# Performance work log

Measured on AMD Instinct MI355X. Metric: run time of the kernel, lower is better.

The kernel has to match this reference:

```python
import jax, jax.numpy as jnp
import numpy as np

B, N, NC, T, C, H = 8, 16, 16, 64, 512, 8


def setup_inputs() -> dict:
    key = jax.random.key(0)
    ks = jax.random.split(key, 7)
    s = 1.0 / np.sqrt(C)  # ~kaiming-uniform scale for Linear weights
    x = jax.random.normal(ks[0], (B, N, T, C), dtype=jnp.float32)
    c = jax.random.normal(ks[1], (B, NC, T, C), dtype=jnp.float32)
    mask = jax.random.randint(ks[2], (B, N * T, (N + NC) * T), 0, 2).astype(bool)
    Wq = jax.random.normal(ks[3], (C, C), dtype=jnp.float32) * s  # [out, in], torch Linear layout
    Wk = jax.random.normal(ks[4], (C, C), dtype=jnp.float32) * s
    Wv = jax.random.normal(ks[5], (C, C), dtype=jnp.float32) * s
    Wp = jax.random.normal(ks[6], (C, C), dtype=jnp.float32) * s
    return {"x": x, "c": c, "mask": mask, "Wq": Wq, "Wk": Wk, "Wv": Wv, "Wp": Wp}


def reference(x, c, mask, Wq, Wk, Wv, Wp):
    Bx, Nx, Tx, Cx = x.shape
    Dh = Cx // H
    kv_in = jnp.concatenate([x, c], axis=1)           # hybrid: [B, N+NC, T, C]
    Nk = kv_in.shape[1]
    # torch Linear: y = x @ W.T  -> einsum '...c,dc->...d'
    q = jnp.einsum('bntc,dc->bntd', x, Wq).reshape(Bx, Nx * Tx, H, Dh).transpose(0, 2, 1, 3)
    k = jnp.einsum('bntc,dc->bntd', kv_in, Wk).reshape(Bx, Nk * Tx, H, Dh).transpose(0, 2, 1, 3)
    v = jnp.einsum('bntc,dc->bntd', kv_in, Wv).reshape(Bx, Nk * Tx, H, Dh).transpose(0, 2, 1, 3)
    att = jnp.einsum('bhqd,bhkd->bhqk', q, k) * (1.0 / np.sqrt(Dh))  # [B,H,NT,NkT]
    att = jnp.where(mask[:, None, :, :], -jnp.inf, att)
    att = jax.nn.softmax(att, axis=-1)
    y = jnp.einsum('bhqk,bhkd->bhqd', att, v)          # [B,H,NT,Dh]
    y = y.transpose(0, 2, 1, 3).reshape(Bx, Nx * Tx, Cx)
    y = jnp.einsum('btc,dc->btd', y, Wp)
    return y.reshape(Bx, Nx, Tx, Cx)
```

## Files before the change

kernel.cpp:

```cpp
#include <hip/hip_runtime.h>
#include <hip/hip_bf16.h>
#include <stdint.h>

typedef __bf16 v8bf __attribute__((ext_vector_type(8)));
typedef short v4s __attribute__((ext_vector_type(4)));
typedef float f32x4 __attribute__((ext_vector_type(4)));

__device__ __forceinline__ void gload_lds16(const void* g, void* l) {
    __builtin_amdgcn_global_load_lds(
        (const __attribute__((address_space(1))) void*)g,
        (__attribute__((address_space(3))) void*)l, 16, 0, 0);
}

__device__ __forceinline__ unsigned short f2bf(float f) {
    __hip_bfloat16 h = __float2bfloat16(f);
    return __builtin_bit_cast(unsigned short, h);
}

__device__ __forceinline__ f32x4 mfma16x16x16bf(v4s a, v4s b, f32x4 c) {
#if __has_builtin(__builtin_amdgcn_mfma_f32_16x16x16bf16_1k)
    return __builtin_amdgcn_mfma_f32_16x16x16bf16_1k(a, b, c, 0, 0, 0);
#elif __has_builtin(__builtin_amdgcn_mfma_f32_16x16x16_bf16)
    return __builtin_amdgcn_mfma_f32_16x16x16_bf16(a, b, c, 0, 0, 0);
#else
    asm("s_nop 1\n\t"
        "v_mfma_f32_16x16x16_bf16 %0, %1, %2, %0\n\t"
        "s_nop 7\n\ts_nop 3"
        : "+v"(c) : "v"(a), "v"(b));
    return c;
#endif
}

__global__ __launch_bounds__(256) void cvt_xcw(const float* __restrict__ x,
                                               const float* __restrict__ c,
                                               const float* __restrict__ wq,
                                               const float* __restrict__ wk,
                                               const float* __restrict__ wv,
                                               const float* __restrict__ wp,
                                               __hip_bfloat16* __restrict__ xc,
                                               __hip_bfloat16* __restrict__ wout) {
    int bid = blockIdx.x;
    if (bid < 8192) {
        int i = bid * 256 + threadIdx.x;
        long e = (long)i * 4;
        int b = (int)(e >> 20);
        int rem = (int)(e & ((1 << 20) - 1));
        int r = rem >> 9;
        int col = rem & 511;
        const float* src = (r < 1024) ? (x + ((long)b << 19) + (long)r * 512 + col)
                                      : (c + ((long)b << 19) + (long)(r - 1024) * 512 + col);
        float4 v = *(const float4*)src;
        ushort4 o;
        o.x = f2bf(v.x); o.y = f2bf(v.y); o.z = f2bf(v.z); o.w = f2bf(v.w);
        ((ushort4*)xc)[i] = o;
    } else {
        int i = (bid - 8192) * 256 + threadIdx.x;
        int e = i * 4;
        int w = e >> 18;
        int off = e & ((1 << 18) - 1);
        const float* src = (w == 0 ? wq : w == 1 ? wk : w == 2 ? wv : wp) + off;
        float4 val = *(const float4*)src;
        ushort4 o;
        o.x = f2bf(val.x); o.y = f2bf(val.y); o.z = f2bf(val.z); o.w = f2bf(val.w);
        ((ushort4*)wout)[i] = o;
    }
}

__global__ __launch_bounds__(256) void cvt_mask(const int* __restrict__ mask,
                                                unsigned long long* __restrict__ mbt) {
    int t = threadIdx.x;
    long base = (long)blockIdx.x * 1024;
#pragma unroll
    for (int j = 0; j < 4; j++) {
        long i = base + j * 256 + t;
        int v = mask[i] != 0;
        unsigned long long bits = __ballot(v);
        if ((t & 63) == 0) {
            int b = (int)(i >> 21);
            int q = (int)((i >> 11) & 1023);
            int word = (int)((i >> 6) & 31);
            mbt[((long)b * 32 + word) * 1024 + q] = bits;
        }
    }
}

__global__ __launch_bounds__(256) void gemm_qkv(const __hip_bfloat16* __restrict__ A,
                                                const __hip_bfloat16* __restrict__ Bw,
                                                __hip_bfloat16* __restrict__ Qw,
                                                __hip_bfloat16* __restrict__ Kw,
                                                __hip_bfloat16* __restrict__ Vtw) {
    __shared__ union {
        struct { __hip_bfloat16 As[128 * 32]; __hip_bfloat16 Bs[128 * 32]; } s;
        __hip_bfloat16 T[128 * 136];
    } u;
    const int tid = threadIdx.x;
    const int wave = tid >> 6, lane = tid & 63;
    const int m0 = blockIdx.x * 128, n0 = blockIdx.y * 128;

    const int la = lane >> 2;
    const int kc = (lane & 3) * 8;
    const long ga0 = (long)(m0 + wave * 16 + la) * 512 + kc;
    const long ga1 = (long)(m0 + (wave + 4) * 16 + la) * 512 + kc;
    const long gb0 = (long)(n0 + wave * 16 + la) * 512 + kc;
    const long gb1 = (long)(n0 + (wave + 4) * 16 + la) * 512 + kc;

    f32x4 acc[4][4] = {};
    const int mw = (wave & 1) * 64, nw = (wave >> 1) * 64;
    const int lrow = lane & 15, lk = (lane >> 4) * 8;

    for (int k0 = 0; k0 < 512; k0 += 32) {
        gload_lds16(A + ga0 + k0, &u.s.As[wave * 512]);
        gload_lds16(A + ga1 + k0, &u.s.As[(wave + 4) * 512]);
        gload_lds16(Bw + gb0 + k0, &u.s.Bs[wave * 512]);
        gload_lds16(Bw + gb1 + k0, &u.s.Bs[(wave + 4) * 512]);
        __syncthreads();
        v8bf a[4], b[4];
#pragma unroll
        for (int i = 0; i < 4; i++) {
            a[i] = *(const v8bf*)&u.s.As[(mw + i * 16 + lrow) * 32 + lk];
            b[i] = *(const v8bf*)&u.s.Bs[(nw + i * 16 + lrow) * 32 + lk];
        }
#pragma unroll
        for (int mi = 0; mi < 4; mi++)
#pragma unroll
            for (int ni = 0; ni < 4; ni++)
                acc[mi][ni] = __builtin_amdgcn_mfma_f32_16x16x32_bf16(a[mi], b[ni], acc[mi][ni], 0, 0, 0);
        __syncthreads();
    }

    const int lq = lane >> 4;
    if (blockIdx.y < 8) {
#pragma unroll
        for (int mi = 0; mi < 4; mi++)
#pragma unroll
            for (int ni = 0; ni < 4; ni++)
#pragma unroll
                for (int r = 0; r < 4; r++) {
                    int grow = m0 + mw + mi * 16 + lq * 4 + r;
                    int gcol = n0 + nw + ni * 16 + lrow;
                    int w = gcol >> 9, g9 = gcol & 511;
                    int h = g9 >> 6, dh = g9 & 63;
                    int b_ = grow >> 11, rr = grow & 2047;
                    float val = acc[mi][ni][r];
                    if (w == 0) {
                        if (rr < 1024)
                            Qw[((long)(b_ * 8 + h) * 1024 + rr) * 64 + dh] =
                                __float2bfloat16(val * 0.1803368801f);
                    } else {
                        Kw[((long)(b_ * 8 + h) * 2048 + rr) * 64 + dh] = __float2bfloat16(val);
                    }
                }
    } else {
#pragma unroll
        for (int mi = 0; mi < 4; mi++)
#pragma unroll
            for (int ni = 0; ni < 4; ni++) {
                int n_l = nw + ni * 16 + lrow;
                int m_l = mw + mi * 16 + lq * 4;
                ushort4 pk;
                pk.x = f2bf(acc[mi][ni][0]); pk.y = f2bf(acc[mi][ni][1]);
                pk.z = f2bf(acc[mi][ni][2]); pk.w = f2bf(acc[mi][ni][3]);
                *(ushort4*)&u.T[n_l * 136 + m_l] = pk;
            }
        __syncthreads();
        const int no = (blockIdx.y - 8) * 128;
        const int b_ = m0 >> 11, rrb = m0 & 2047;
#pragma unroll
        for (int i = 0; i < 8; i++) {
            int s = tid + i * 256;
            int n_l = s >> 4, ch = s & 15;
            int ng = no + n_l;
            int h = ng >> 6, dh = ng & 63;
            uint4 v = *(const uint4*)&u.T[n_l * 136 + ch * 8];
            *(uint4*)&Vtw[((long)(b_ * 8 + h) * 64 + dh) * 2048 + rrb + ch * 8] = v;
        }
    }
}

__global__ __launch_bounds__(256) void gemm_out(const __hip_bfloat16* __restrict__ A,
                                                const __hip_bfloat16* __restrict__ Bw,
                                                float* __restrict__ outp) {
    __shared__ __hip_bfloat16 As[128 * 32];
    __shared__ __hip_bfloat16 Bs[128 * 32];
    const int tid = threadIdx.x;
    const int wave = tid >> 6, lane = tid & 63;
    const int m0 = blockIdx.x * 128, n0 = blockIdx.y * 128;

    const int la = lane >> 2;
    const int kc = (lane & 3) * 8;
    const long ga0 = (long)(m0 + wave * 16 + la) * 512 + kc;
    const long ga1 = (long)(m0 + (wave + 4) * 16 + la) * 512 + kc;
    const long gb0 = (long)(n0 + wave * 16 + la) * 512 + kc;
    const long gb1 = (long)(n0 + (wave + 4) * 16 + la) * 512 + kc;

    f32x4 acc[4][4] = {};
    const int mw = (wave & 1) * 64, nw = (wave >> 1) * 64;
    const int lrow = lane & 15, lk = (lane >> 4) * 8;

    for (int k0 = 0; k0 < 512; k0 += 32) {
        gload_lds16(A + ga0 + k0, &As[wave * 512]);
        gload_lds16(A + ga1 + k0, &As[(wave + 4) * 512]);
        gload_lds16(Bw + gb0 + k0, &Bs[wave * 512]);
        gload_lds16(Bw + gb1 + k0, &Bs[(wave + 4) * 512]);
        __syncthreads();
        v8bf a[4], b[4];
#pragma unroll
        for (int i = 0; i < 4; i++) {
            a[i] = *(const v8bf*)&As[(mw + i * 16 + lrow) * 32 + lk];
            b[i] = *(const v8bf*)&Bs[(nw + i * 16 + lrow) * 32 + lk];
        }
#pragma unroll
        for (int mi = 0; mi < 4; mi++)
#pragma unroll
            for (int ni = 0; ni < 4; ni++)
                acc[mi][ni] = __builtin_amdgcn_mfma_f32_16x16x32_bf16(a[mi], b[ni], acc[mi][ni], 0, 0, 0);
        __syncthreads();
    }

    const int lq = lane >> 4;
#pragma unroll
    for (int mi = 0; mi < 4; mi++)
#pragma unroll
        for (int ni = 0; ni < 4; ni++)
#pragma unroll
            for (int r = 0; r < 4; r++) {
                int grow = m0 + mw + mi * 16 + lq * 4 + r;
                int gcol = n0 + nw + ni * 16 + lrow;
                outp[(long)grow * 512 + gcol] = acc[mi][ni][r];
            }
}

__global__ __launch_bounds__(256) void flash(const __hip_bfloat16* __restrict__ Q,
                                             const __hip_bfloat16* __restrict__ K,
                                             const __hip_bfloat16* __restrict__ Vt,
                                             const unsigned long long* __restrict__ Mbt,
                                             __hip_bfloat16* __restrict__ Y) {
    constexpr int LDT = 72;
    __shared__ __hip_bfloat16 Ks[64 * LDT];
    __shared__ __hip_bfloat16 Vts[64 * LDT];

    const int L = blockIdx.x;
    const int b = L & 7, qt = (L >> 3) & 15, h = L >> 7;
    const int bh = b * 8 + h;
    const int tid = threadIdx.x, w = tid >> 6, lane = tid & 63;
    const int lcol = lane & 15, lq = lane >> 4;

    const __hip_bfloat16* Qp = Q + ((long)bh * 1024 + qt * 64 + w * 16 + lcol) * 64 + lq * 8;
    const __hip_bfloat16* Kg = K + (long)bh * 2048 * 64;
    const __hip_bfloat16* Vg = Vt + (long)bh * 64 * 2048;
    const unsigned long long* Mp = Mbt + (long)b * 32 * 1024 + qt * 64 + w * 16 + lcol;

    v8bf bq0 = *(const v8bf*)(Qp);
    v8bf bq1 = *(const v8bf*)(Qp + 32);

    f32x4 O[4] = {};
    float lsum = 0.f;

    for (int kt = 0; kt < 32; kt++) {
        unsigned long long mword = Mp[(long)kt * 1024];
        const uint4* ksrc = (const uint4*)(Kg + kt * 64 * 64);
#pragma unroll
        for (int i = 0; i < 2; i++) {
            int u = tid + i * 256, r = u >> 3, part = u & 7;
            *(uint4*)&Ks[r * LDT + part * 8] = ksrc[u];
        }
#pragma unroll
        for (int i = 0; i < 2; i++) {
            int u = tid + i * 256, dh = u >> 3, part = u & 7;
            *(uint4*)&Vts[dh * LDT + part * 8] = *(const uint4*)(Vg + (long)dh * 2048 + kt * 64 + part * 8);
        }
        __syncthreads();

#pragma unroll
        for (int nt = 0; nt < 4; nt++) {
            v8bf ak0 = *(const v8bf*)&Ks[(nt * 16 + lcol) * LDT + lq * 8];
            v8bf ak1 = *(const v8bf*)&Ks[(nt * 16 + lcol) * LDT + 32 + lq * 8];
            f32x4 st = {};
            st = __builtin_amdgcn_mfma_f32_16x16x32_bf16(ak0, bq0, st, 0, 0, 0);
            st = __builtin_amdgcn_mfma_f32_16x16x32_bf16(ak1, bq1, st, 0, 0, 0);
            unsigned int nib = (unsigned int)(mword >> (nt * 16 + lq * 4)) & 0xFu;
            float e0 = ((nib >> 0) & 1u) ? 0.f : __builtin_amdgcn_exp2f(fminf(st[0], 57.f));
            float e1 = ((nib >> 1) & 1u) ? 0.f : __builtin_amdgcn_exp2f(fminf(st[1], 57.f));
            float e2 = ((nib >> 2) & 1u) ? 0.f : __builtin_amdgcn_exp2f(fminf(st[2], 57.f));
            float e3 = ((nib >> 3) & 1u) ? 0.f : __builtin_amdgcn_exp2f(fminf(st[3], 57.f));
            lsum += (e0 + e1) + (e2 + e3);
            __hip_bfloat162 lo = __float22bfloat162_rn(make_float2(e0, e1));
            __hip_bfloat162 hi = __float22bfloat162_rn(make_float2(e2, e3));
            uint2 pku;
            __builtin_memcpy(&pku.x, &lo, 4);
            __builtin_memcpy(&pku.y, &hi, 4);
            v4s pa = __builtin_bit_cast(v4s, pku);
#pragma unroll
            for (int nd = 0; nd < 4; nd++) {
                v4s bv = *(const v4s*)&Vts[(nd * 16 + lcol) * LDT + nt * 16 + lq * 4];
                O[nd] = mfma16x16x16bf(pa, bv, O[nd]);
            }
        }
        __syncthreads();
    }

    float s = lsum;
    s += __shfl_xor(s, 16);
    s += __shfl_xor(s, 32);
    float inv[4];
#pragma unroll
    for (int r = 0; r < 4; r++) inv[r] = 1.f / __shfl(s, lq * 4 + r);

    __hip_bfloat16* Yp = Y + ((long)b * 1024 + qt * 64 + w * 16) * 512 + h * 64 + lcol;
#pragma unroll
    for (int nd = 0; nd < 4; nd++)
#pragma unroll
        for (int r = 0; r < 4; r++)
            Yp[(long)(lq * 4 + r) * 512 + nd * 16] = __float2bfloat16(O[nd][r] * inv[r]);
}

extern "C" void kernel_launch(void* const* d_in, const int* in_sizes, int n_in,
                              void* d_out, int out_size, void* d_ws, size_t ws_size,
                              hipStream_t stream) {
    const float* x = (const float*)d_in[0];
    const float* c = (const float*)d_in[1];
    const int* mask = (const int*)d_in[2];
    const float* Wq = (const float*)d_in[3];
    const float* Wk = (const float*)d_in[4];
    const float* Wv = (const float*)d_in[5];
    const float* Wp = (const float*)d_in[6];

    char* ws = (char*)d_ws;
    __hip_bfloat16* xc  = (__hip_bfloat16*)(ws);
    __hip_bfloat16* Wbf = (__hip_bfloat16*)(ws + 16777216);
    __hip_bfloat16* Qw  = (__hip_bfloat16*)(ws + 18874368);
    __hip_bfloat16* Kw  = (__hip_bfloat16*)(ws + 27262976);
    __hip_bfloat16* Vtw = (__hip_bfloat16*)(ws + 44040192);
    __hip_bfloat16* Yb  = (__hip_bfloat16*)(ws + 60817408);
    unsigned long long* Mbp = (unsigned long long*)(ws);

    cvt_xcw<<<9216, 256, 0, stream>>>(x, c, Wq, Wk, Wv, Wp, xc, Wbf);
    gemm_qkv<<<dim3(128, 12), 256, 0, stream>>>(xc, Wbf, Qw, Kw, Vtw);
    cvt_mask<<<16384, 256, 0, stream>>>(mask, Mbp);
    flash<<<1024, 256, 0, stream>>>(Qw, Kw, Vtw, Mbp, Yb);
    gemm_out<<<dim3(64, 4), 256, 0, stream>>>(Yb, Wbf + 3 * 262144, (float*)d_out);
}
```

Baseline: 285.7 us.

## Double-buffer K/V tiles in flash kernel with register prefetch and MFMA priority

Loads for the next K and V^T tile are issued into registers before computing on the current tile, then written to the alternate LDS buffer after compute, with one barrier per iteration instead of two. This aims to hide global-load latency behind the MFMA and exp work. It also wraps MFMA sections in s_setprio to favor matrix issue across waves. Costs are doubled LDS use and extra registers held across the loop, which may reduce occupancy.

```diff
diff --git a/kernel.cpp b/kernel.cpp
--- a/kernel.cpp
+++ b/kernel.cpp
@@ -236,8 +236,8 @@
                                              const unsigned long long* __restrict__ Mbt,
                                              __hip_bfloat16* __restrict__ Y) {
     constexpr int LDT = 72;
-    __shared__ __hip_bfloat16 Ks[64 * LDT];
-    __shared__ __hip_bfloat16 Vts[64 * LDT];
+    __shared__ __hip_bfloat16 Ks[2][64 * LDT];
+    __shared__ __hip_bfloat16 Vts[2][64 * LDT];
 
     const int L = blockIdx.x;
     const int b = L & 7, qt = (L >> 3) & 15, h = L >> 7;
@@ -250,34 +250,52 @@
     const __hip_bfloat16* Vg = Vt + (long)bh * 64 * 2048;
     const unsigned long long* Mp = Mbt + (long)b * 32 * 1024 + qt * 64 + w * 16 + lcol;
 
+    const int u0 = tid, u1 = tid + 256;
+    const int r0 = u0 >> 3, p0 = u0 & 7;
+    const int r1 = u1 >> 3, p1 = u1 & 7;
+
     v8bf bq0 = *(const v8bf*)(Qp);
     v8bf bq1 = *(const v8bf*)(Qp + 32);
 
     f32x4 O[4] = {};
     float lsum = 0.f;
 
+    {
+        const uint4* ksrc = (const uint4*)Kg;
+        uint4 k0 = ksrc[u0], k1 = ksrc[u1];
+        uint4 v0 = *(const uint4*)(Vg + (long)r0 * 2048 + p0 * 8);
+        uint4 v1 = *(const uint4*)(Vg + (long)r1 * 2048 + p1 * 8);
+        *(uint4*)&Ks[0][r0 * LDT + p0 * 8] = k0;
+        *(uint4*)&Ks[0][r1 * LDT + p1 * 8] = k1;
+        *(uint4*)&Vts[0][r0 * LDT + p0 * 8] = v0;
+        *(uint4*)&Vts[0][r1 * LDT + p1 * 8] = v1;
+    }
+    __syncthreads();
+
+    int cur = 0;
     for (int kt = 0; kt < 32; kt++) {
         unsigned long long mword = Mp[(long)kt * 1024];
-        const uint4* ksrc = (const uint4*)(Kg + kt * 64 * 64);
-#pragma unroll
-        for (int i = 0; i < 2; i++) {
-            int u = tid + i * 256, r = u >> 3, part = u & 7;
-            *(uint4*)&Ks[r * LDT + part * 8] = ksrc[u];
-        }
-#pragma unroll
-        for (int i = 0; i < 2; i++) {
-            int u = tid + i * 256, dh = u >> 3, part = u & 7;
-            *(uint4*)&Vts[dh * LDT + part * 8] = *(const uint4*)(Vg + (long)dh * 2048 + kt * 64 + part * 8);
-        }
-        __syncthreads();
-
+
+        uint4 nk0, nk1, nv0, nv1;
+        if (kt < 31) {
+            const uint4* ksrc = (const uint4*)(Kg + ((kt + 1) << 12));
+            nk0 = ksrc[u0];
+            nk1 = ksrc[u1];
+            nv0 = *(const uint4*)(Vg + (long)r0 * 2048 + (kt + 1) * 64 + p0 * 8);
+            nv1 = *(const uint4*)(Vg + (long)r1 * 2048 + (kt + 1) * 64 + p1 * 8);
+        }
+
+        const __hip_bfloat16* Kb = Ks[cur];
+        const __hip_bfloat16* Vb = Vts[cur];
 #pragma unroll
         for (int nt = 0; nt < 4; nt++) {
-            v8bf ak0 = *(const v8bf*)&Ks[(nt * 16 + lcol) * LDT + lq * 8];
-            v8bf ak1 = *(const v8bf*)&Ks[(nt * 16 + lcol) * LDT + 32 + lq * 8];
+            v8bf ak0 = *(const v8bf*)&Kb[(nt * 16 + lcol) * LDT + lq * 8];
+            v8bf ak1 = *(const v8bf*)&Kb[(nt * 16 + lcol) * LDT + 32 + lq * 8];
             f32x4 st = {};
+            __builtin_amdgcn_s_setprio(1);
             st = __builtin_amdgcn_mfma_f32_16x16x32_bf16(ak0, bq0, st, 0, 0, 0);
             st = __builtin_amdgcn_mfma_f32_16x16x32_bf16(ak1, bq1, st, 0, 0, 0);
+            __builtin_amdgcn_s_setprio(0);
             unsigned int nib = (unsigned int)(mword >> (nt * 16 + lq * 4)) & 0xFu;
             float e0 = ((nib >> 0) & 1u) ? 0.f : __builtin_amdgcn_exp2f(fminf(st[0], 57.f));
             float e1 = ((nib >> 1) & 1u) ? 0.f : __builtin_amdgcn_exp2f(fminf(st[1], 57.f));
@@ -290,13 +308,25 @@
             __builtin_memcpy(&pku.x, &lo, 4);
             __builtin_memcpy(&pku.y, &hi, 4);
             v4s pa = __builtin_bit_cast(v4s, pku);
+            __builtin_amdgcn_s_setprio(1);
 #pragma unroll
             for (int nd = 0; nd < 4; nd++) {
-                v4s bv = *(const v4s*)&Vts[(nd * 16 + lcol) * LDT + nt * 16 + lq * 4];
+                v4s bv = *(const v4s*)&Vb[(nd * 16 + lcol) * LDT + nt * 16 + lq * 4];
                 O[nd] = mfma16x16x16bf(pa, bv, O[nd]);
             }
-        }
-        __syncthreads();
+            __builtin_amdgcn_s_setprio(0);
+        }
+
+        if (kt < 31) {
+            __hip_bfloat16* Kw_ = Ks[cur ^ 1];
+            __hip_bfloat16* Vw_ = Vts[cur ^ 1];
+            *(uint4*)&Kw_[r0 * LDT + p0 * 8] = nk0;
+            *(uint4*)&Kw_[r1 * LDT + p1 * 8] = nk1;
+            *(uint4*)&Vw_[r0 * LDT + p0 * 8] = nv0;
+            *(uint4*)&Vw_[r1 * LDT + p1 * 8] = nv1;
+        }
+        __syncthreads();
+        cur ^= 1;
     }
 
     float s = lsum;
```

Measured after the change: 281.0 us. Within noise of the previous version (-1.6%).
